# Kernel tuning notes

Measured on AMD Instinct MI355X. Metric: run time of the kernel, lower is better.

Reference implementation:

```python
import jax, jax.numpy as jnp
import numpy as np

B, S, H, L, NH, HD, V, FF, NC = 8, 512, 768, 12, 12, 64, 21128, 3072, 6
MAX_REL = 64
EPS = 1e-12


def rel_pos_table(seq_len, depth=HD, max_rel=MAX_REL):
    # NeZha functional (sinusoidal) relative-position embeddings, [S, S, depth]
    r = np.arange(seq_len)
    dist = np.clip(r[None, :] - r[:, None], -max_rel, max_rel) + max_rel
    vocab = 2 * max_rel + 1
    pos = np.arange(vocab)[:, None].astype(np.float32)
    i = np.arange(depth)[None, :]
    angle = pos / np.power(10000.0, (2 * (i // 2)) / float(depth))
    table = np.where(i % 2 == 0, np.sin(angle), np.cos(angle)).astype(np.float32)
    return jnp.asarray(table[dist])


def layer_norm(x, g, b):
    mu = jnp.mean(x, axis=-1, keepdims=True)
    var = jnp.mean(jnp.square(x - mu), axis=-1, keepdims=True)
    return (x - mu) * jax.lax.rsqrt(var + EPS) * g + b


def setup_inputs() -> dict:
    key = jax.random.key(0)
    ks = jax.random.split(key, 32)
    sd = 0.02
    d = {
        'input_ids': jax.random.randint(ks[0], (B, S), 0, V, dtype=jnp.int32),
        'attention_mask': jnp.ones((B, S), dtype=jnp.int32),
        'word_emb': sd * jax.random.normal(ks[1], (V, H), jnp.float32),
        'pos_emb': sd * jax.random.normal(ks[2], (S, H), jnp.float32),
        'type_emb': sd * jax.random.normal(ks[3], (2, H), jnp.float32),
        'ln_emb_g': jnp.ones((H,), jnp.float32),
        'ln_emb_b': jnp.zeros((H,), jnp.float32),
        'Wq': sd * jax.random.normal(ks[4], (L, H, H), jnp.float32),
        'bq': jnp.zeros((L, H), jnp.float32),
        'Wk': sd * jax.random.normal(ks[5], (L, H, H), jnp.float32),
        'bk': jnp.zeros((L, H), jnp.float32),
        'Wv': sd * jax.random.normal(ks[6], (L, H, H), jnp.float32),
        'bv': jnp.zeros((L, H), jnp.float32),
        'Wo': sd * jax.random.normal(ks[7], (L, H, H), jnp.float32),
        'bo': jnp.zeros((L, H), jnp.float32),
        'ln1_g': jnp.ones((L, H), jnp.float32),
        'ln1_b': jnp.zeros((L, H), jnp.float32),
        'W1': sd * jax.random.normal(ks[8], (L, H, FF), jnp.float32),
        'b1': jnp.zeros((L, FF), jnp.float32),
        'W2': sd * jax.random.normal(ks[9], (L, FF, H), jnp.float32),
        'b2': jnp.zeros((L, H), jnp.float32),
        'ln2_g': jnp.ones((L, H), jnp.float32),
        'ln2_b': jnp.zeros((L, H), jnp.float32),
        'pool_W': sd * jax.random.normal(ks[10], (H, H), jnp.float32),
        'pool_b': jnp.zeros((H,), jnp.float32),
        'cls_W': sd * jax.random.normal(ks[11], (2 * H, NC), jnp.float32),
        'cls_b': jnp.zeros((NC,), jnp.float32),
    }
    return d


def nezha_forward(input_ids, attention_mask, word_emb, pos_emb, type_emb,
                  ln_emb_g, ln_emb_b, Wq, bq, Wk, bk, Wv, bv, Wo, bo,
                  ln1_g, ln1_b, W1, b1, W2, b2, ln2_g, ln2_b,
                  pool_W, pool_b, cls_W, cls_b):
    seq = input_ids.shape[1]
    rel = rel_pos_table(seq)  # [S, S, HD], shared for keys and values
    mask_bias = (1.0 - attention_mask.astype(jnp.float32)) * -10000.0  # [B, S]

    x = word_emb[input_ids] + pos_emb[:seq][None, :, :] + type_emb[0][None, None, :]
    x = layer_norm(x, ln_emb_g, ln_emb_b)

    scale = 1.0 / jnp.sqrt(jnp.asarray(HD, jnp.float32))
    for l in range(L):
        q = (x @ Wq[l] + bq[l]).reshape(B, seq, NH, HD)
        k = (x @ Wk[l] + bk[l]).reshape(B, seq, NH, HD)
        v = (x @ Wv[l] + bv[l]).reshape(B, seq, NH, HD)
        # content scores + relative-position key scores
        scores = jnp.einsum('bihd,bjhd->bhij', q, k) + jnp.einsum('bihd,ijd->bhij', q, rel)
        scores = scores * scale + mask_bias[:, None, None, :]
        attn = jax.nn.softmax(scores, axis=-1)
        # content context + relative-position value context
        ctx = jnp.einsum('bhij,bjhd->bihd', attn, v) + jnp.einsum('bhij,ijd->bihd', attn, rel)
        ctx = ctx.reshape(B, seq, H)
        x = layer_norm(x + ctx @ Wo[l] + bo[l], ln1_g[l], ln1_b[l])
        h = jax.nn.gelu(x @ W1[l] + b1[l], approximate=False)
        x = layer_norm(x + h @ W2[l] + b2[l], ln2_g[l], ln2_b[l])

    pooled = jnp.tanh(x[:, 0] @ pool_W + pool_b)        # [B, H]
    seq_avg = jnp.mean(x, axis=1)                        # [B, H] (unmasked, as in torch.mean)
    concat = jnp.concatenate([seq_avg, pooled], axis=1)  # [B, 2H]
    return concat @ cls_W + cls_b                        # [B, 6]


def reference(input_ids, attention_mask, word_emb, pos_emb, type_emb,
              ln_emb_g, ln_emb_b, Wq, bq, Wk, bk, Wv, bv, Wo, bo,
              ln1_g, ln1_b, W1, b1, W2, b2, ln2_g, ln2_b,
              pool_W, pool_b, cls_W, cls_b):
    return nezha_forward(input_ids, attention_mask, word_emb, pos_emb, type_emb,
                         ln_emb_g, ln_emb_b, Wq, bq, Wk, bk, Wv, bv, Wo, bo,
                         ln1_g, ln1_b, W1, b1, W2, b2, ln2_g, ln2_b,
                         pool_W, pool_b, cls_W, cls_b)
```

## Files before the change

### kernel.cpp

```cpp
#include <hip/hip_runtime.h>
#include <hip/hip_bf16.h>
#include <math.h>

typedef __hip_bfloat16 bf;

#define B_ 8
#define S_ 512
#define H_ 768
#define L_ 12
#define NH_ 12
#define HD_ 64
#define FF_ 3072
#define NC_ 6
#define BS_ (B_ * S_)
#define BSH_ ((size_t)BS_ * H_)
#define KAUG_ 672
#define TAUG_ 160
#define TPAD_ 144
#define QSTR_ 2304

typedef __attribute__((ext_vector_type(8))) short s16x8;
typedef __attribute__((ext_vector_type(4))) float fx4;

__device__ __forceinline__ float LD(const void* p, size_t i, int isbf) {
    return isbf ? __bfloat162float(((const bf*)p)[i]) : ((const float*)p)[i];
}

__device__ __forceinline__ void gload16(const void* g, void* l) {
    __builtin_amdgcn_global_load_lds(
        (const __attribute__((address_space(1))) void*)g,
        (__attribute__((address_space(3))) void*)l, 16, 0, 0);
}

__device__ __forceinline__ s16x8 ldfrag64(const unsigned short* base, int row, int chunk) {
    return *(const s16x8*)((const char*)base + row * 128 + ((chunk ^ (row & 7)) << 4));
}
__device__ __forceinline__ s16x8 ldfrag32(const unsigned short* base, int row, int chunk) {
    return *(const s16x8*)((const char*)base + row * 64 + ((chunk ^ (row & 3)) << 4));
}

__device__ __forceinline__ float wred_sum(float v) {
#pragma unroll
    for (int o = 32; o; o >>= 1) v += __shfl_xor(v, o, 64);
    return v;
}
__device__ __forceinline__ float wred_max(float v) {
#pragma unroll
    for (int o = 32; o; o >>= 1) v = fmaxf(v, __shfl_xor(v, o, 64));
    return v;
}

__global__ void detect_kernel(const unsigned int* __restrict__ g, int* __restrict__ flag) {
    if (threadIdx.x == 0 && blockIdx.x == 0) {
        flag[0] = (g[0] == 0x3F800000u) ? 0 : 1;
        flag[1] = 0;
    }
}

__global__ void build_table_kernel(float* __restrict__ tab) {
    int idx = blockIdx.x * 256 + threadIdx.x;
    if (idx >= 129 * 64) return;
    int p = idx >> 6, d = idx & 63;
    double angle = (double)p / pow(10000.0, (double)(2 * (d / 2)) / 64.0);
    tab[idx] = (float)((d & 1) ? cos(angle) : sin(angle));
}

__global__ void build_tabT_kernel(const float* __restrict__ tab,
                                  bf* __restrict__ th, bf* __restrict__ tl) {
    int idx = blockIdx.x * 256 + threadIdx.x;
    if (idx >= 64 * TAUG_) return;
    int d = idx / TAUG_, t = idx % TAUG_;
    float v = (t < 129) ? tab[t * 64 + d] : 0.0f;
    bf h = __float2bfloat16(v);
    th[idx] = h;
    tl[idx] = __float2bfloat16(v - __bfloat162float(h));
}

__global__ void build_tabS_kernel(const float* __restrict__ tab,
                                  bf* __restrict__ th, bf* __restrict__ tl) {
    int idx = blockIdx.x * 256 + threadIdx.x;
    if (idx >= TPAD_ * 64) return;
    int t = idx >> 6;
    float v = (t < 129) ? tab[idx] : 0.0f;
    bf h = __float2bfloat16(v);
    th[idx] = h;
    tl[idx] = __float2bfloat16(v - __bfloat162float(h));
}

__global__ __launch_bounds__(256) void embed_kernel(
    const int* __restrict__ ids, const void* __restrict__ we,
    const void* __restrict__ pe, const void* __restrict__ te,
    float* __restrict__ y, const int* __restrict__ fl) {
    int isbf = *fl;
    int t = blockIdx.x;
    int s = t & (S_ - 1);
    int id = ids[t];
    size_t base = (size_t)t * H_;
    for (int c = threadIdx.x; c < H_; c += 256) {
        y[base + c] = LD(we, (size_t)id * H_ + c, isbf) +
                      LD(pe, (size_t)s * H_ + c, isbf) +
                      LD(te, c, isbf);
    }
}

__global__ void maskbias_kernel(const int* __restrict__ mask, float* __restrict__ mb) {
    int t = blockIdx.x * 256 + threadIdx.x;
    if (t < BS_) mb[t] = (1.0f - (float)mask[t]) * -10000.0f;
}

__global__ void biascat_kernel(const void* __restrict__ bq, const void* __restrict__ bk,
                               const void* __restrict__ bv, size_t off,
                               float* __restrict__ out, const int* __restrict__ fl) {
    int isbf = *fl;
    int t = blockIdx.x * 256 + threadIdx.x;
    if (t >= 3 * H_) return;
    const void* src = t < H_ ? bq : (t < 2 * H_ ? bk : bv);
    out[t] = LD(src, off + (t % H_), isbf);
}

__global__ __launch_bounds__(256) void ln_kernel(
    float* out, bf* ohi, bf* olo, const float* a, const float* resid,
    const void* __restrict__ g, const void* __restrict__ b, size_t goff,
    const int* __restrict__ fl) {
    const int isbf = *fl;
    const int lane = threadIdx.x & 63, wv = threadIdx.x >> 6;
    const int row = blockIdx.x * 4 + wv;
    const size_t base = (size_t)row * H_;
    float v[12];
#pragma unroll
    for (int e = 0; e < 12; ++e) {
        const int c = lane + e * 64;
        v[e] = a[base + c];
        if (resid) v[e] += resid[base + c];
    }
    float s = 0.0f;
#pragma unroll
    for (int e = 0; e < 12; ++e) s += v[e];
    const float mu = wred_sum(s) * (1.0f / (float)H_);
    float q = 0.0f;
#pragma unroll
    for (int e = 0; e < 12; ++e) { v[e] -= mu; q += v[e] * v[e]; }
    const float rs = 1.0f / sqrtf(wred_sum(q) * (1.0f / (float)H_) + 1e-12f);
#pragma unroll
    for (int e = 0; e < 12; ++e) {
        const int c = lane + e * 64;
        float o = v[e] * rs * LD(g, goff + c, isbf) + LD(b, goff + c, isbf);
        out[base + c] = o;
        if (ohi) {
            bf h = __float2bfloat16(o);
            ohi[base + c] = h;
            olo[base + c] = __float2bfloat16(o - __bfloat162float(h));
        }
    }
}

__global__ __launch_bounds__(256) void transpose_split_kernel(
    const void* __restrict__ W, size_t woff, bf* __restrict__ th, bf* __restrict__ tl,
    int K, int N, const int* __restrict__ fl) {
    __shared__ float s[32][33];
    const int isbf = *fl;
    const int tx = threadIdx.x & 31, ty = threadIdx.x >> 5;
    const int k0 = blockIdx.x * 32, n0 = blockIdx.y * 32;
#pragma unroll
    for (int i = 0; i < 4; ++i) {
        int k = k0 + ty + i * 8;
        s[ty + i * 8][tx] = LD(W, woff + (size_t)k * N + (n0 + tx), isbf);
    }
    __syncthreads();
#pragma unroll
    for (int i = 0; i < 4; ++i) {
        int n = n0 + ty + i * 8;
        float v = s[tx][ty + i * 8];
        bf h = __float2bfloat16(v);
        bf l = __float2bfloat16(v - __bfloat162float(h));
        th[(size_t)n * K + k0 + tx] = h;
        tl[(size_t)n * K + k0 + tx] = l;
    }
}

template<int MR>
__global__ __launch_bounds__(256, 2) void mgemm_kernel(
    const bf* __restrict__ Ah, const bf* __restrict__ Al,
    const bf* __restrict__ Bh, const bf* __restrict__ Bl,
    const void* __restrict__ bias, size_t boff,
    float* __restrict__ C, bf* __restrict__ Chi, bf* __restrict__ Clo,
    int N, int K, int act, int split_out, const int* __restrict__ fl) {
    __shared__ __align__(16) unsigned short Ahs[MR * 32][32];
    __shared__ __align__(16) unsigned short Als[MR * 32][32];
    __shared__ __align__(16) unsigned short Bhs[128][32];
    __shared__ __align__(16) unsigned short Bls[128][32];
    const int tid  = threadIdx.x;
    const int lane = tid & 63;
    const int wid  = tid >> 6;
    const int wr   = wid >> 1, wc = wid & 1;
    const int m0 = blockIdx.y * (MR * 32), n0 = blockIdx.x * 128;
    const int srow = lane >> 2;
    const int scol = (lane & 3) * 8;

    const fx4 fzero = {0.f, 0.f, 0.f, 0.f};
    fx4 acc[MR][4];
#pragma unroll
    for (int i = 0; i < MR; ++i)
#pragma unroll
        for (int j = 0; j < 4; ++j) acc[i][j] = fzero;

    for (int k0 = 0; k0 < K; k0 += 32) {
#pragma unroll
        for (int t = 0; t < MR / 2; ++t) {
            const int r = wid * (MR * 8) + t * 16;
            const size_t ga = (size_t)(m0 + r + srow) * K + (k0 + scol);
            gload16(Ah + ga, &Ahs[r][0]);
            gload16(Al + ga, &Als[r][0]);
        }
#pragma unroll
        for (int t = 0; t < 2; ++t) {
            const int r = wid * 32 + t * 16;
            const size_t gb = (size_t)(n0 + r + srow) * K + (k0 + scol);
            gload16(Bh + gb, &Bhs[r][0]);
            gload16(Bl + gb, &Bls[r][0]);
        }
        __syncthreads();

        const int fr = lane & 15;
        const int ko = (lane >> 4) * 8;
        s16x8 ah[MR], al[MR], bh[4], bl[4];
#pragma unroll
        for (int f = 0; f < MR; ++f) {
            ah[f] = *(const s16x8*)&Ahs[wr * (MR * 16) + f * 16 + fr][ko];
            al[f] = *(const s16x8*)&Als[wr * (MR * 16) + f * 16 + fr][ko];
        }
#pragma unroll
        for (int f = 0; f < 4; ++f) {
            bh[f] = *(const s16x8*)&Bhs[wc * 64 + f * 16 + fr][ko];
            bl[f] = *(const s16x8*)&Bls[wc * 64 + f * 16 + fr][ko];
        }
#pragma unroll
        for (int im = 0; im < MR; ++im)
#pragma unroll
            for (int in = 0; in < 4; ++in) {
                acc[im][in] = __builtin_amdgcn_mfma_f32_16x16x32_bf16(ah[im], bh[in], acc[im][in], 0, 0, 0);
                acc[im][in] = __builtin_amdgcn_mfma_f32_16x16x32_bf16(ah[im], bl[in], acc[im][in], 0, 0, 0);
                acc[im][in] = __builtin_amdgcn_mfma_f32_16x16x32_bf16(al[im], bh[in], acc[im][in], 0, 0, 0);
            }
        __syncthreads();
    }

    const int isbf = *fl;
    const int cr0 = m0 + wr * (MR * 16) + (lane >> 4) * 4;
    const int cc0 = n0 + wc * 64 + (lane & 15);
#pragma unroll
    for (int in = 0; in < 4; ++in) {
        const int col = cc0 + in * 16;
        const float bv = LD(bias, boff + col, isbf);
#pragma unroll
        for (int im = 0; im < MR; ++im) {
#pragma unroll
            for (int r = 0; r < 4; ++r) {
                const int row = cr0 + im * 16 + r;
                float v = acc[im][in][r] + bv;
                if (act) v = 0.5f * v * (1.0f + erff(v * 0.70710678118654752f));
                if (split_out) {
                    bf h = __float2bfloat16(v);
                    bf l = __float2bfloat16(v - __bfloat162float(h));
                    Chi[(size_t)row * N + col] = h;
                    Clo[(size_t)row * N + col] = l;
                } else {
                    C[(size_t)row * N + col] = v;
                }
            }
        }
    }
}

__global__ __launch_bounds__(256) void qrel_kernel(
    const bf* __restrict__ qh, const bf* __restrict__ ql,
    const bf* __restrict__ tabSh, const bf* __restrict__ tabSl,
    float* __restrict__ qrel, int astr, int b0) {
    const int tid = threadIdx.x, lane = tid & 63, wv = tid >> 6;
    const int rbase = blockIdx.x * 128;
    const int h = blockIdx.y;
    const int t0 = blockIdx.z * 48;
    const int fr = lane & 15, ko = (lane >> 4) * 8;
    const fx4 fz = {0.f, 0.f, 0.f, 0.f};
    fx4 acc[2][3];
#pragma unroll
    for (int m = 0; m < 2; ++m)
#pragma unroll
        for (int n = 0; n < 3; ++n) acc[m][n] = fz;
#pragma unroll
    for (int ks = 0; ks < 2; ++ks) {
        s16x8 a_h[2], a_l[2], b_h[3], b_l[3];
#pragma unroll
        for (int m = 0; m < 2; ++m) {
            const int row = rbase + wv * 32 + m * 16 + fr;
            const size_t ga = ((size_t)(b0 * S_) + row) * astr + h * 64 + ks * 32 + ko;
            a_h[m] = *(const s16x8*)(qh + ga);
            a_l[m] = *(const s16x8*)(ql + ga);
        }
#pragma unroll
        for (int n = 0; n < 3; ++n) {
            const int trow = t0 + n * 16 + fr;
            const size_t gb = (size_t)trow * 64 + ks * 32 + ko;
            b_h[n] = *(const s16x8*)(tabSh + gb);
            b_l[n] = *(const s16x8*)(tabSl + gb);
        }
#pragma unroll
        for (int m = 0; m < 2; ++m)
#pragma unroll
            for (int n = 0; n < 3; ++n) {
                acc[m][n] = __builtin_amdgcn_mfma_f32_16x16x32_bf16(a_h[m], b_h[n], acc[m][n], 0, 0, 0);
                acc[m][n] = __builtin_amdgcn_mfma_f32_16x16x32_bf16(a_h[m], b_l[n], acc[m][n], 0, 0, 0);
                acc[m][n] = __builtin_amdgcn_mfma_f32_16x16x32_bf16(a_l[m], b_h[n], acc[m][n], 0, 0, 0);
            }
    }
    const int rr = (lane >> 4) * 4, cc = lane & 15;
#pragma unroll
    for (int m = 0; m < 2; ++m)
#pragma unroll
        for (int n = 0; n < 3; ++n)
#pragma unroll
            for (int r = 0; r < 4; ++r) {
                const int row = rbase + wv * 32 + m * 16 + rr + r;
                const int t = t0 + n * 16 + cc;
                const int bb = row >> 9, ii = row & (S_ - 1);
                qrel[(((size_t)bb * NH_ + h) * S_ + ii) * TPAD_ + t] = acc[m][n][r];
            }
}

__global__ __launch_bounds__(256, 2) void qk_kernel(
    const bf* __restrict__ qh, const bf* __restrict__ ql,
    const bf* __restrict__ kh, const bf* __restrict__ kl,
    float* __restrict__ sc, int astr, int b0) {
    __shared__ __align__(16) unsigned short Qh[128][64];
    __shared__ __align__(16) unsigned short Ql_[128][64];
    __shared__ __align__(16) unsigned short Kh[128][64];
    __shared__ __align__(16) unsigned short Kl[128][64];
    const int tid = threadIdx.x, lane = tid & 63, wv = tid >> 6;
    const int j0 = blockIdx.x * 128, i0 = blockIdx.y * 128;
    const int h = blockIdx.z % NH_, bb = blockIdx.z / NH_;
    const int b = b0 + bb;
    const int srow = lane >> 3;
    const int schunk = (lane & 7) ^ (srow & 7);
#pragma unroll
    for (int t = 0; t < 4; ++t) {
        const int r = wv * 32 + t * 8;
        const size_t ga = (size_t)(b * S_ + i0 + r + srow) * astr + h * 64 + schunk * 8;
        const size_t gb = (size_t)(b * S_ + j0 + r + srow) * astr + h * 64 + schunk * 8;
        gload16(qh + ga, &Qh[r][0]);
        gload16(ql + ga, &Ql_[r][0]);
        gload16(kh + gb, &Kh[r][0]);
        gload16(kl + gb, &Kl[r][0]);
    }
    __syncthreads();
    const int fr = lane & 15, g = lane >> 4;
    const int wr = wv >> 1, wc = wv & 1;
    const fx4 fz = {0.f, 0.f, 0.f, 0.f};
    fx4 acc[4][4];
#pragma unroll
    for (int i = 0; i < 4; ++i)
#pragma unroll
        for (int j = 0; j < 4; ++j) acc[i][j] = fz;
#pragma unroll
    for (int ks = 0; ks < 2; ++ks) {
        s16x8 ah[4], al[4], bh[4], bl[4];
#pragma unroll
        for (int m = 0; m < 4; ++m) {
            const int row = wr * 64 + m * 16 + fr;
            ah[m] = ldfrag64(&Qh[0][0], row, ks * 4 + g);
            al[m] = ldfrag64(&Ql_[0][0], row, ks * 4 + g);
        }
#pragma unroll
        for (int n = 0; n < 4; ++n) {
            const int row = wc * 64 + n * 16 + fr;
            bh[n] = ldfrag64(&Kh[0][0], row, ks * 4 + g);
            bl[n] = ldfrag64(&Kl[0][0], row, ks * 4 + g);
        }
#pragma unroll
        for (int m = 0; m < 4; ++m)
#pragma unroll
            for (int n = 0; n < 4; ++n) {
                acc[m][n] = __builtin_amdgcn_mfma_f32_16x16x32_bf16(ah[m], bh[n], acc[m][n], 0, 0, 0);
                acc[m][n] = __builtin_amdgcn_mfma_f32_16x16x32_bf16(ah[m], bl[n], acc[m][n], 0, 0, 0);
                acc[m][n] = __builtin_amdgcn_mfma_f32_16x16x32_bf16(al[m], bh[n], acc[m][n], 0, 0, 0);
            }
    }
    const int rr = (lane >> 4) * 4, cc = lane & 15;
#pragma unroll
    for (int m = 0; m < 4; ++m)
#pragma unroll
        for (int n = 0; n < 4; ++n)
#pragma unroll
            for (int r = 0; r < 4; ++r) {
                const int ii = i0 + wr * 64 + m * 16 + rr + r;
                const int jj = j0 + wc * 64 + n * 16 + cc;
                sc[(((size_t)bb * NH_ + h) * S_ + ii) * S_ + jj] = acc[m][n][r];
            }
}

__global__ __launch_bounds__(256) void smrel_kernel(
    const float* __restrict__ scores, const float* __restrict__ qrel,
    const float* __restrict__ mb,
    bf* __restrict__ pah, bf* __restrict__ pal, int b0) {
    const int lane = threadIdx.x & 63;
    const int wv = threadIdx.x >> 6;
    const int i = blockIdx.x * 4 + wv;
    const int h = blockIdx.y, bb = blockIdx.z;
    const int b = b0 + bb;
    const size_t srow = ((size_t)bb * NH_ + h) * S_ + i;
    const size_t qbase = srow * TPAD_;

    float s[8];
    float lmax = -1e30f;
#pragma unroll
    for (int rep = 0; rep < 8; ++rep) {
        const int j = lane + rep * 64;
        int t = j - i; t = t < -64 ? -64 : (t > 64 ? 64 : t);
        float v = (scores[srow * S_ + j] + qrel[qbase + t + 64]) * 0.125f + mb[b * S_ + j];
        s[rep] = v;
        lmax = fmaxf(lmax, v);
    }
    const float mx = wred_max(lmax);
    float lsum = 0.0f;
#pragma unroll
    for (int rep = 0; rep < 8; ++rep) {
        s[rep] = expf(s[rep] - mx);
        lsum += s[rep];
    }
    const float inv = 1.0f / wred_sum(lsum);

    const size_t rowbase = srow * KAUG_;
#pragma unroll
    for (int e = 0; e < 3; ++e) {
        const int t = lane + e * 64;
        if (t < TAUG_) {
            pah[rowbase + 512 + t] = __float2bfloat16(0.0f);
            pal[rowbase + 512 + t] = __float2bfloat16(0.0f);
        }
    }
    float s_lo = 0.0f, s_hi = 0.0f;
#pragma unroll
    for (int rep = 0; rep < 8; ++rep) {
        const int j = lane + rep * 64;
        const float v = s[rep] * inv;
        bf hh = __float2bfloat16(v);
        pah[rowbase + j] = hh;
        pal[rowbase + j] = __float2bfloat16(v - __bfloat162float(hh));
        const int d = j - i;
        if (d <= -64) s_lo += s[rep];
        else if (d >= 64) s_hi += s[rep];
        else {
            pah[rowbase + 512 + d + 64] = hh;
            pal[rowbase + 512 + d + 64] = __float2bfloat16(v - __bfloat162float(hh));
        }
    }
    s_lo = wred_sum(s_lo);
    s_hi = wred_sum(s_hi);
    if (lane == 0) {
        float v0 = s_lo * inv;
        bf h0 = __float2bfloat16(v0);
        pah[rowbase + 512] = h0;
        pal[rowbase + 512] = __float2bfloat16(v0 - __bfloat162float(h0));
        float v1 = s_hi * inv;
        bf h1 = __float2bfloat16(v1);
        pah[rowbase + 512 + 128] = h1;
        pal[rowbase + 512 + 128] = __float2bfloat16(v1 - __bfloat162float(h1));
    }
}

__global__ __launch_bounds__(256) void vaug_kernel(
    const bf* __restrict__ vh, const bf* __restrict__ vl,
    const bf* __restrict__ tabTh, const bf* __restrict__ tabTl,
    bf* __restrict__ vah, bf* __restrict__ val_, int astr, int b0) {
    __shared__ unsigned short tile[64][71];
    const int h = blockIdx.x, pl = blockIdx.y, bb = blockIdx.z;
    const int b = b0 + bb;
    const bf* src  = pl ? vl : vh;
    bf*       dst  = pl ? val_ : vah;
    const bf* tsrc = pl ? tabTl : tabTh;
    const int tid = threadIdx.x;
    const size_t dbase = ((size_t)bb * NH_ + h) * 64;
    for (int j0 = 0; j0 < S_; j0 += 64) {
        for (int idx = tid; idx < 4096; idx += 256) {
            int jj = idx >> 6, d = idx & 63;
            tile[jj][d] = *(const unsigned short*)&src[(size_t)(b * S_ + j0 + jj) * astr + h * 64 + d];
        }
        __syncthreads();
        for (int idx = tid; idx < 4096; idx += 256) {
            int d = idx >> 6, jj = idx & 63;
            *(unsigned short*)&dst[(dbase + d) * KAUG_ + j0 + jj] = tile[jj][d];
        }
        __syncthreads();
    }
    for (int idx = tid; idx < 64 * TAUG_; idx += 256) {
        int d = idx / TAUG_, t = idx % TAUG_;
        *(unsigned short*)&dst[(dbase + d) * KAUG_ + 512 + t] =
            *(const unsigned short*)&tsrc[idx];
    }
}

__global__ __launch_bounds__(256, 2) void pv_kernel(
    const bf* __restrict__ pah, const bf* __restrict__ pal,
    const bf* __restrict__ vah, const bf* __restrict__ val_,
    bf* __restrict__ ch, bf* __restrict__ cl, int b0) {
    __shared__ __align__(16) unsigned short Ah[128][32];
    __shared__ __align__(16) unsigned short Al[128][32];
    __shared__ __align__(16) unsigned short Bh[64][32];
    __shared__ __align__(16) unsigned short Bl[64][32];
    const int tid = threadIdx.x, lane = tid & 63, wv = tid >> 6;
    const int h = blockIdx.x, i0 = blockIdx.y * 128, bb = blockIdx.z;
    const int b = b0 + bb;
    const int srow = lane >> 2;
    const int schunk = (lane & 3) ^ (srow & 3);
    const fx4 fz = {0.f, 0.f, 0.f, 0.f};
    fx4 acc[2][4];
#pragma unroll
    for (int m = 0; m < 2; ++m)
#pragma unroll
        for (int n = 0; n < 4; ++n) acc[m][n] = fz;

    for (int k0 = 0; k0 < KAUG_; k0 += 32) {
#pragma unroll
        for (int t = 0; t < 2; ++t) {
            const int r = wv * 32 + t * 16;
            const size_t ga = (((size_t)bb * NH_ + h) * S_ + i0 + r + srow) * KAUG_ + k0 + schunk * 8;
            gload16(pah + ga, &Ah[r][0]);
            gload16(pal + ga, &Al[r][0]);
        }
        {
            const int r = wv * 16;
            const size_t gb = (((size_t)bb * NH_ + h) * 64 + r + srow) * KAUG_ + k0 + schunk * 8;
            gload16(vah + gb, &Bh[r][0]);
            gload16(val_ + gb, &Bl[r][0]);
        }
        __syncthreads();
        const int fr = lane & 15, g = lane >> 4;
        s16x8 a_h[2], a_l[2], b_h[4], b_l[4];
#pragma unroll
        for (int m = 0; m < 2; ++m) {
            const int row = wv * 32 + m * 16 + fr;
            a_h[m] = ldfrag32(&Ah[0][0], row, g);
            a_l[m] = ldfrag32(&Al[0][0], row, g);
        }
#pragma unroll
        for (int n = 0; n < 4; ++n) {
            const int row = n * 16 + fr;
            b_h[n] = ldfrag32(&Bh[0][0], row, g);
            b_l[n] = ldfrag32(&Bl[0][0], row, g);
        }
// ... 29 lines not shown
    const void* __restrict__ pb, float* __restrict__ pooled,
    const int* __restrict__ fl) {
    int isbf = *fl;
    int b = blockIdx.x;
    const float* xr = x + (size_t)b * S_ * H_;
    for (int n = threadIdx.x; n < H_; n += 256) {
        float acc = LD(pb, n, isbf);
        for (int kx = 0; kx < H_; ++kx)
            acc += xr[kx] * LD(pW, (size_t)kx * H_ + n, isbf);
        pooled[b * H_ + n] = tanhf(acc);
    }
}

__global__ __launch_bounds__(256) void seqavg_kernel(
    const float* __restrict__ x, float* __restrict__ sa) {
    int b = blockIdx.x;
    for (int c = threadIdx.x; c < H_; c += 256) {
        float s = 0.0f;
        for (int j = 0; j < S_; ++j) s += x[((size_t)b * S_ + j) * H_ + c];
        sa[b * H_ + c] = s * (1.0f / (float)S_);
    }
}

__global__ void head_kernel(const float* __restrict__ sa, const float* __restrict__ pooled,
                            const void* __restrict__ cW, const void* __restrict__ cb,
                            void* __restrict__ out, const int* __restrict__ fl) {
    int isbf = *fl;
    int t = threadIdx.x;
    if (t >= B_ * NC_) return;
    int b = t / NC_, c = t % NC_;
    float acc = LD(cb, c, isbf);
    for (int kx = 0; kx < H_; ++kx)
        acc += sa[b * H_ + kx] * LD(cW, (size_t)kx * NC_ + c, isbf);
    for (int kx = 0; kx < H_; ++kx)
        acc += pooled[b * H_ + kx] * LD(cW, (size_t)(H_ + kx) * NC_ + c, isbf);
    if (isbf) ((bf*)out)[t] = __float2bfloat16(acc);
    else      ((float*)out)[t] = acc;
}

extern "C" void kernel_launch(void* const* d_in, const int* in_sizes, int n_in,
                              void* d_out, int out_size, void* d_ws, size_t ws_size,
                              hipStream_t stream) {
    (void)in_sizes; (void)n_in; (void)out_size;
    const int* ids   = (const int*)d_in[0];
    const int* amask = (const int*)d_in[1];
    const void* we  = d_in[2];
    const void* pe  = d_in[3];
    const void* te  = d_in[4];
    const void* lng = d_in[5];
    const void* lnb = d_in[6];
    const void* Wq  = d_in[7];
    const void* bq  = d_in[8];
    const void* Wk  = d_in[9];
    const void* bk  = d_in[10];
    const void* Wv  = d_in[11];
    const void* bv  = d_in[12];
    const void* Wo  = d_in[13];
    const void* bo  = d_in[14];
    const void* l1g = d_in[15];
    const void* l1b = d_in[16];
    const void* W1  = d_in[17];
    const void* b1  = d_in[18];
    const void* W2  = d_in[19];
    const void* b2  = d_in[20];
    const void* l2g = d_in[21];
    const void* l2b = d_in[22];
    const void* pW  = d_in[23];
    const void* pb  = d_in[24];
    const void* cW  = d_in[25];
    const void* cb  = d_in[26];

    char* cur = (char*)d_ws;
    auto alloc = [&](size_t bytes) -> char* {
        char* p = cur;
        cur += (bytes + 255) & ~(size_t)255;
        return p;
    };
    float* x    = (float*)alloc(BSH_ * 4);
    float* r0   = (float*)alloc(BSH_ * 4);
    float* r1f  = (float*)alloc(BSH_ * 4);
    float* r2f  = (float*)alloc(BSH_ * 4);
    float* r3f  = (float*)alloc(BSH_ * 4);
    float* z    = (float*)alloc(BSH_ * 4);
    float* tab  = (float*)alloc(129 * 64 * 4);
    float* mb   = (float*)alloc(BS_ * 4);
    float* pool = (float*)alloc(B_ * H_ * 4);
    float* sa   = (float*)alloc(B_ * H_ * 4);
    float* bqkv = (float*)alloc(3 * H_ * 4);
    bf* tabTh   = (bf*)alloc(64 * TAUG_ * 2);
    bf* tabTl   = (bf*)alloc(64 * TAUG_ * 2);
    bf* tabSh   = (bf*)alloc(TPAD_ * 64 * 2);
    bf* tabSl   = (bf*)alloc(TPAD_ * 64 * 2);
    int* flag   = (int*)alloc(256);
    int* zflag  = flag + 1;

    const size_t fixed = (size_t)(cur - (char*)d_ws);
    auto regA_sz = [&](int CB) {
        size_t wt = (size_t)2 * H_ * FF_ * 2;
        size_t qr = (size_t)CB * NH_ * S_ * TPAD_ * 4;
        return (wt > qr ? wt : qr);
    };
    auto regB_sz = [&](int CB) {
        size_t xs = (size_t)4 * BSH_;
        size_t sc = (size_t)CB * NH_ * S_ * S_ * 4;
        return (xs > sc ? xs : sc);
    };
    auto need = [&](int CB) {
        return fixed + regA_sz(CB) + regB_sz(CB)
             + (size_t)CB * NH_ * S_ * KAUG_ * 2 * 2
             + (size_t)CB * NH_ * 64 * KAUG_ * 2 * 2
             + 4096;
    };
    int CB = 8;
    while (CB > 1 && need(CB) > ws_size) CB >>= 1;

    char* regA = alloc(regA_sz(CB));
    char* regB = alloc(regB_sz(CB));
    bf* pah  = (bf*)alloc((size_t)CB * NH_ * S_ * KAUG_ * 2 * 2);
    bf* pal  = pah + (size_t)CB * NH_ * S_ * KAUG_;
    bf* vah  = (bf*)alloc((size_t)CB * NH_ * 64 * KAUG_ * 2 * 2);
    bf* val_ = vah + (size_t)CB * NH_ * 64 * KAUG_;

    bf*    wth   = (bf*)regA;
    bf*    wtl   = wth + (size_t)H_ * FF_;
    float* qrelb = (float*)regA;
    bf*    xh    = (bf*)regB;
    bf*    xl    = xh + BSH_;
    float* scb   = (float*)regB;

    bf* qkvh = (bf*)r1f;
    bf* qkvl = qkvh + (size_t)BS_ * QSTR_;
    bf* ch   = (bf*)r0;  bf* cl = ch + BSH_;
    bf* hbh  = (bf*)r0;
    bf* hbl  = (bf*)r2f;

    detect_kernel<<<1, 64, 0, stream>>>((const unsigned int*)lng, flag);
    build_table_kernel<<<(129 * 64 + 255) / 256, 256, 0, stream>>>(tab);
    build_tabT_kernel<<<(64 * TAUG_ + 255) / 256, 256, 0, stream>>>(tab, tabTh, tabTl);
    build_tabS_kernel<<<(TPAD_ * 64 + 255) / 256, 256, 0, stream>>>(tab, tabSh, tabSl);
    maskbias_kernel<<<(BS_ + 255) / 256, 256, 0, stream>>>(amask, mb);
    embed_kernel<<<BS_, 256, 0, stream>>>(ids, we, pe, te, r0, flag);
    ln_kernel<<<BS_ / 4, 256, 0, stream>>>(x, xh, xl, r0, nullptr, lng, lnb, 0, flag);

    dim3 tpHH(H_ / 32, H_ / 32);
    dim3 tpHF(H_ / 32, FF_ / 32);
    dim3 tpFH(FF_ / 32, H_ / 32);
    dim3 gQKV(3 * H_ / 128, BS_ / 128);
    dim3 gH64(H_ / 128, BS_ / 64);
    dim3 gF(FF_ / 128, BS_ / 128);
    dim3 gQR(CB * S_ / 128, NH_, 3);
    dim3 gVA(NH_, 2, CB);
    dim3 gQK(4, 4, NH_ * CB);
    dim3 gSM(S_ / 4, NH_, CB);
    dim3 gPV(NH_, 4, CB);

    for (int l = 0; l < L_; ++l) {
        const size_t oHH = (size_t)l * H_ * H_;
        const size_t oH  = (size_t)l * H_;
        const size_t oHF = (size_t)l * H_ * FF_;
        const size_t oF  = (size_t)l * FF_;

        transpose_split_kernel<<<tpHH, 256, 0, stream>>>(Wq, oHH, wth, wtl, H_, H_, flag);
        transpose_split_kernel<<<tpHH, 256, 0, stream>>>(Wk, oHH,
            wth + (size_t)H_ * H_, wtl + (size_t)H_ * H_, H_, H_, flag);
        transpose_split_kernel<<<tpHH, 256, 0, stream>>>(Wv, oHH,
            wth + (size_t)2 * H_ * H_, wtl + (size_t)2 * H_ * H_, H_, H_, flag);
        biascat_kernel<<<(3 * H_ + 255) / 256, 256, 0, stream>>>(bq, bk, bv, oH, bqkv, flag);
        mgemm_kernel<4><<<gQKV, 256, 0, stream>>>(xh, xl, wth, wtl, bqkv, 0,
            nullptr, qkvh, qkvl, QSTR_, H_, 0, 1, zflag);

        for (int b0 = 0; b0 < B_; b0 += CB) {
            qrel_kernel<<<gQR, 256, 0, stream>>>(qkvh, qkvl, tabSh, tabSl, qrelb, QSTR_, b0);
            vaug_kernel<<<gVA, 256, 0, stream>>>(qkvh + 2 * H_, qkvl + 2 * H_,
                tabTh, tabTl, vah, val_, QSTR_, b0);
            qk_kernel<<<gQK, 256, 0, stream>>>(qkvh, qkvl, qkvh + H_, qkvl + H_,
                scb, QSTR_, b0);
            smrel_kernel<<<gSM, 256, 0, stream>>>(scb, qrelb, mb, pah, pal, b0);
            pv_kernel<<<gPV, 256, 0, stream>>>(pah, pal, vah, val_, ch, cl, b0);
        }

        transpose_split_kernel<<<tpHH, 256, 0, stream>>>(Wo, oHH, wth, wtl, H_, H_, flag);
        mgemm_kernel<2><<<gH64, 256, 0, stream>>>(ch, cl, wth, wtl, bo, oH,
            z, nullptr, nullptr, H_, H_, 0, 0, flag);
        ln_kernel<<<BS_ / 4, 256, 0, stream>>>(x, xh, xl, z, x, l1g, l1b, oH, flag);

        transpose_split_kernel<<<tpHF, 256, 0, stream>>>(W1, oHF, wth, wtl, H_, FF_, flag);
        mgemm_kernel<4><<<gF, 256, 0, stream>>>(xh, xl, wth, wtl, b1, oF,
            nullptr, hbh, hbl, FF_, H_, 1, 1, flag);
        transpose_split_kernel<<<tpFH, 256, 0, stream>>>(W2, oHF, wth, wtl, FF_, H_, flag);
        mgemm_kernel<2><<<gH64, 256, 0, stream>>>(hbh, hbl, wth, wtl, b2, oH,
            z, nullptr, nullptr, H_, FF_, 0, 0, flag);
        ln_kernel<<<BS_ / 4, 256, 0, stream>>>(x, xh, xl, z, x, l2g, l2b, oH, flag);
    }

    pool_kernel<<<B_, 256, 0, stream>>>(x, pW, pb, pool, flag);
    seqavg_kernel<<<B_, 256, 0, stream>>>(x, sa);
    head_kernel<<<1, 64, 0, stream>>>(sa, pool, cW, cb, d_out, flag);
}
```

Baseline: 6.869 ms.

## Fuse QK scores with softmax, split-K output GEMMs, swizzle GEMM blocks

Merges the QK score kernel and the relative-position softmax kernel into one kernel that keeps a full 128x512 score tile in registers, so the fp32 score matrix is never written to and read back from global memory. Output-projection and FFN-down GEMMs switch to a two-way split-K with 128-row tiles, and the two partial sums are added inside the following layernorm. GEMM workgroups are swizzled. The Q/K/V transposes are batched into a single launch, and all layers' biases are concatenated once up front. The fused kernel needs 128KB of dynamic LDS and large register arrays at occupancy 1, and split-K adds an extra fp32 buffer read.

```diff
diff --git a/kernel.cpp b/kernel.cpp
--- a/kernel.cpp
+++ b/kernel.cpp
@@ -44,9 +44,15 @@
     for (int o = 32; o; o >>= 1) v += __shfl_xor(v, o, 64);
     return v;
 }
-__device__ __forceinline__ float wred_max(float v) {
-#pragma unroll
-    for (int o = 32; o; o >>= 1) v = fmaxf(v, __shfl_xor(v, o, 64));
+
+__device__ __forceinline__ float gred_max(float v) {
+#pragma unroll
+    for (int o = 1; o < 16; o <<= 1) v = fmaxf(v, __shfl_xor(v, o, 64));
+    return v;
+}
+__device__ __forceinline__ float gred_sum(float v) {
+#pragma unroll
+    for (int o = 1; o < 16; o <<= 1) v += __shfl_xor(v, o, 64);
     return v;
 }
 
@@ -109,17 +115,18 @@
 }
 
 __global__ void biascat_kernel(const void* __restrict__ bq, const void* __restrict__ bk,
-                               const void* __restrict__ bv, size_t off,
-                               float* __restrict__ out, const int* __restrict__ fl) {
+                               const void* __restrict__ bv, float* __restrict__ out,
+                               const int* __restrict__ fl) {
     int isbf = *fl;
     int t = blockIdx.x * 256 + threadIdx.x;
-    if (t >= 3 * H_) return;
-    const void* src = t < H_ ? bq : (t < 2 * H_ ? bk : bv);
-    out[t] = LD(src, off + (t % H_), isbf);
+    if (t >= L_ * 3 * H_) return;
+    int l = t / (3 * H_), p = t % (3 * H_);
+    const void* s = p < H_ ? bq : (p < 2 * H_ ? bk : bv);
+    out[t] = LD(s, (size_t)l * H_ + (p % H_), isbf);
 }
 
 __global__ __launch_bounds__(256) void ln_kernel(
-    float* out, bf* ohi, bf* olo, const float* a, const float* resid,
+    float* out, bf* ohi, bf* olo, const float* a, const float* a2, const float* resid,
     const void* __restrict__ g, const void* __restrict__ b, size_t goff,
     const int* __restrict__ fl) {
     const int isbf = *fl;
@@ -131,6 +138,7 @@
     for (int e = 0; e < 12; ++e) {
         const int c = lane + e * 64;
         v[e] = a[base + c];
+        if (a2) v[e] += a2[base + c];
         if (resid) v[e] += resid[base + c];
     }
     float s = 0.0f;
@@ -178,22 +186,59 @@
     }
 }
 
+__global__ __launch_bounds__(256) void transpose_split3_kernel(
+    const void* __restrict__ W0, const void* __restrict__ W1p, const void* __restrict__ W2p,
+    size_t woff, bf* __restrict__ th, bf* __restrict__ tl, const int* __restrict__ fl) {
+    __shared__ float s[32][33];
+    const int isbf = *fl;
+    const void* W = blockIdx.z == 0 ? W0 : (blockIdx.z == 1 ? W1p : W2p);
+    bf* tho = th + (size_t)blockIdx.z * H_ * H_;
+    bf* tlo = tl + (size_t)blockIdx.z * H_ * H_;
+    const int tx = threadIdx.x & 31, ty = threadIdx.x >> 5;
+    const int k0 = blockIdx.x * 32, n0 = blockIdx.y * 32;
+#pragma unroll
+    for (int i = 0; i < 4; ++i) {
+        int k = k0 + ty + i * 8;
+        s[ty + i * 8][tx] = LD(W, woff + (size_t)k * H_ + (n0 + tx), isbf);
+    }
+    __syncthreads();
+#pragma unroll
+    for (int i = 0; i < 4; ++i) {
+        int n = n0 + ty + i * 8;
+        float v = s[tx][ty + i * 8];
+        bf h = __float2bfloat16(v);
+        bf l = __float2bfloat16(v - __bfloat162float(h));
+        tho[(size_t)n * H_ + k0 + tx] = h;
+        tlo[(size_t)n * H_ + k0 + tx] = l;
+    }
+}
+
 template<int MR>
 __global__ __launch_bounds__(256, 2) void mgemm_kernel(
     const bf* __restrict__ Ah, const bf* __restrict__ Al,
     const bf* __restrict__ Bh, const bf* __restrict__ Bl,
     const void* __restrict__ bias, size_t boff,
-    float* __restrict__ C, bf* __restrict__ Chi, bf* __restrict__ Clo,
-    int N, int K, int act, int split_out, const int* __restrict__ fl) {
+    float* __restrict__ C, float* __restrict__ C2,
+    bf* __restrict__ Chi, bf* __restrict__ Clo,
+    int N, int K, int lda, int ldb, int act, int split_out, const int* __restrict__ fl) {
     __shared__ __align__(16) unsigned short Ahs[MR * 32][32];
     __shared__ __align__(16) unsigned short Als[MR * 32][32];
     __shared__ __align__(16) unsigned short Bhs[128][32];
     __shared__ __align__(16) unsigned short Bls[128][32];
+    const int gx = gridDim.x, gy = gridDim.y, gz = gridDim.z;
+    const int nwg = gx * gy * gz;
+    const int flat = (blockIdx.z * gy + blockIdx.y) * gx + blockIdx.x;
+    const int swz = (flat & 7) * (nwg >> 3) + (flat >> 3);
+    const int bx = swz % gx;
+    const int by = (swz / gx) % gy;
+    const int bz = swz / (gx * gy);
+
     const int tid  = threadIdx.x;
     const int lane = tid & 63;
     const int wid  = tid >> 6;
     const int wr   = wid >> 1, wc = wid & 1;
-    const int m0 = blockIdx.y * (MR * 32), n0 = blockIdx.x * 128;
+    const int m0 = by * (MR * 32), n0 = bx * 128;
+    const size_t koff = (size_t)bz * K;
     const int srow = lane >> 2;
     const int scol = (lane & 3) * 8;
 
@@ -208,14 +253,14 @@
 #pragma unroll
         for (int t = 0; t < MR / 2; ++t) {
             const int r = wid * (MR * 8) + t * 16;
-            const size_t ga = (size_t)(m0 + r + srow) * K + (k0 + scol);
+            const size_t ga = (size_t)(m0 + r + srow) * lda + koff + k0 + scol;
             gload16(Ah + ga, &Ahs[r][0]);
             gload16(Al + ga, &Als[r][0]);
         }
 #pragma unroll
         for (int t = 0; t < 2; ++t) {
             const int r = wid * 32 + t * 16;
-            const size_t gb = (size_t)(n0 + r + srow) * K + (k0 + scol);
+            const size_t gb = (size_t)(n0 + r + srow) * ldb + koff + k0 + scol;
             gload16(Bh + gb, &Bhs[r][0]);
             gload16(Bl + gb, &Bls[r][0]);
         }
@@ -246,12 +291,13 @@
     }
 
     const int isbf = *fl;
+    float* Co = (bz == 0) ? C : C2;
     const int cr0 = m0 + wr * (MR * 16) + (lane >> 4) * 4;
     const int cc0 = n0 + wc * 64 + (lane & 15);
 #pragma unroll
     for (int in = 0; in < 4; ++in) {
         const int col = cc0 + in * 16;
-        const float bv = LD(bias, boff + col, isbf);
+        const float bv = (bz == 0) ? LD(bias, boff + col, isbf) : 0.0f;
 #pragma unroll
         for (int im = 0; im < MR; ++im) {
 #pragma unroll
@@ -265,7 +311,7 @@
                     Chi[(size_t)row * N + col] = h;
                     Clo[(size_t)row * N + col] = l;
                 } else {
-                    C[(size_t)row * N + col] = v;
+                    Co[(size_t)row * N + col] = v;
                 }
             }
         }
@@ -327,143 +373,181 @@
             }
 }
 
-__global__ __launch_bounds__(256, 2) void qk_kernel(
+__global__ __launch_bounds__(512, 1) void qksm_kernel(
     const bf* __restrict__ qh, const bf* __restrict__ ql,
     const bf* __restrict__ kh, const bf* __restrict__ kl,
-    float* __restrict__ sc, int astr, int b0) {
-    __shared__ __align__(16) unsigned short Qh[128][64];
-    __shared__ __align__(16) unsigned short Ql_[128][64];
-    __shared__ __align__(16) unsigned short Kh[128][64];
-    __shared__ __align__(16) unsigned short Kl[128][64];
+    const float* __restrict__ qrel, const float* __restrict__ mb,
+    bf* __restrict__ pah, bf* __restrict__ pal, int astr, int b0) {
+    extern __shared__ __align__(16) char smem[];
+    unsigned short (*Kh_)[64] = (unsigned short(*)[64])smem;
+    unsigned short (*Kl_)[64] = (unsigned short(*)[64])(smem + 65536);
+    unsigned short (*P_)[512] = (unsigned short(*)[512])smem;
+    __shared__ float st_m[2][128], st_s[2][128], st_lo[2][128], st_hi[2][128];
+
     const int tid = threadIdx.x, lane = tid & 63, wv = tid >> 6;
-    const int j0 = blockIdx.x * 128, i0 = blockIdx.y * 128;
-    const int h = blockIdx.z % NH_, bb = blockIdx.z / NH_;
+    const int i0 = blockIdx.x * 128, h = blockIdx.y, bb = blockIdx.z;
     const int b = b0 + bb;
-    const int srow = lane >> 3;
-    const int schunk = (lane & 7) ^ (srow & 7);
-#pragma unroll
-    for (int t = 0; t < 4; ++t) {
-        const int r = wv * 32 + t * 8;
-        const size_t ga = (size_t)(b * S_ + i0 + r + srow) * astr + h * 64 + schunk * 8;
-        const size_t gb = (size_t)(b * S_ + j0 + r + srow) * astr + h * 64 + schunk * 8;
-        gload16(qh + ga, &Qh[r][0]);
-        gload16(ql + ga, &Ql_[r][0]);
-        gload16(kh + gb, &Kh[r][0]);
-        gload16(kl + gb, &Kl[r][0]);
-    }
+    const int rg = wv >> 1, hf = wv & 1;
+
+    const int srow = lane >> 3, schunk = (lane & 7) ^ (srow & 7);
+#pragma unroll
+    for (int t = 0; t < 8; ++t) {
+        const int r = wv * 64 + t * 8;
+        const size_t ga = (size_t)(b * S_ + r + srow) * astr + h * 64 + schunk * 8;
+        gload16(kh + ga, &Kh_[r][0]);
+        gload16(kl + ga, &Kl_[r][0]);
+    }
+    const int fr = lane & 15, gq = lane >> 4;
+    s16x8 a_h[2][2], a_l[2][2];
+#pragma unroll
+    for (int mm = 0; mm < 2; ++mm)
+#pragma unroll
+        for (int ks = 0; ks < 2; ++ks) {
+            const size_t ga = (size_t)(b * S_ + i0 + rg * 32 + mm * 16 + fr) * astr
+                            + h * 64 + ks * 32 + gq * 8;
+            a_h[mm][ks] = *(const s16x8*)(qh + ga);
+            a_l[mm][ks] = *(const s16x8*)(ql + ga);
+        }
     __syncthreads();
-    const int fr = lane & 15, g = lane >> 4;
-    const int wr = wv >> 1, wc = wv & 1;
+
     const fx4 fz = {0.f, 0.f, 0.f, 0.f};
-    fx4 acc[4][4];
-#pragma unroll
-    for (int i = 0; i < 4; ++i)
-#pragma unroll
-        for (int j = 0; j < 4; ++j) acc[i][j] = fz;
-#pragma unroll
-    for (int ks = 0; ks < 2; ++ks) {
-        s16x8 ah[4], al[4], bh[4], bl[4];
-#pragma unroll
-        for (int m = 0; m < 4; ++m) {
-            const int row = wr * 64 + m * 16 + fr;
-            ah[m] = ldfrag64(&Qh[0][0], row, ks * 4 + g);
-            al[m] = ldfrag64(&Ql_[0][0], row, ks * 4 + g);
-        }
-#pragma unroll
-        for (int n = 0; n < 4; ++n) {
-            const int row = wc * 64 + n * 16 + fr;
-            bh[n] = ldfrag64(&Kh[0][0], row, ks * 4 + g);
-            bl[n] = ldfrag64(&Kl[0][0], row, ks * 4 + g);
-        }
-#pragma unroll
-        for (int m = 0; m < 4; ++m)
-#pragma unroll
-            for (int n = 0; n < 4; ++n) {
-                acc[m][n] = __builtin_amdgcn_mfma_f32_16x16x32_bf16(ah[m], bh[n], acc[m][n], 0, 0, 0);
-                acc[m][n] = __builtin_amdgcn_mfma_f32_16x16x32_bf16(ah[m], bl[n], acc[m][n], 0, 0, 0);
-                acc[m][n] = __builtin_amdgcn_mfma_f32_16x16x32_bf16(al[m], bh[n], acc[m][n], 0, 0, 0);
-            }
-    }
-    const int rr = (lane >> 4) * 4, cc = lane & 15;
-#pragma unroll
-    for (int m = 0; m < 4; ++m)
-#pragma unroll
-        for (int n = 0; n < 4; ++n)
+    fx4 acc[2][16];
+#pragma unroll
+    for (int m = 0; m < 2; ++m)
+#pragma unroll
+        for (int n = 0; n < 16; ++n) acc[m][n] = fz;
+#pragma unroll
+    for (int nn = 0; nn < 16; ++nn) {
+        const int jrow = hf * 256 + nn * 16 + fr;
+#pragma unroll
+        for (int ks = 0; ks < 2; ++ks) {
+            const s16x8 b_h = ldfrag64(&Kh_[0][0], jrow, ks * 4 + gq);
+            const s16x8 b_l = ldfrag64(&Kl_[0][0], jrow, ks * 4 + gq);
+#pragma unroll
+            for (int mm = 0; mm < 2; ++mm) {
+                acc[mm][nn] = __builtin_amdgcn_mfma_f32_16x16x32_bf16(a_h[mm][ks], b_h, acc[mm][nn], 0, 0, 0);
+                acc[mm][nn] = __builtin_amdgcn_mfma_f32_16x16x32_bf16(a_h[mm][ks], b_l, acc[mm][nn], 0, 0, 0);
+                acc[mm][nn] = __builtin_amdgcn_mfma_f32_16x16x32_bf16(a_l[mm][ks], b_h, acc[mm][nn], 0, 0, 0);
+            }
+        }
+    }
+
+    const int c = lane & 15;
+    float m_w[2][4];
+#pragma unroll
+    for (int mm = 0; mm < 2; ++mm) {
+#pragma unroll
+        for (int r = 0; r < 4; ++r) {
+            const int row_l = rg * 32 + mm * 16 + gq * 4 + r;
+            const int ig = i0 + row_l;
+            const size_t qb = (((size_t)bb * NH_ + h) * S_ + ig) * TPAD_;
+            const float q0 = qrel[qb], q128 = qrel[qb + 128];
+            float mx = -1e30f;
+#pragma unroll
+            for (int nn = 0; nn < 16; ++nn) {
+                const int j = hf * 256 + nn * 16 + c;
+                const int d = j - ig;
+                const float qr = d <= -64 ? q0 : (d >= 64 ? q128 : qrel[qb + d + 64]);
+                const float v = (acc[mm][nn][r] + qr) * 0.125f + mb[b * S_ + j];
+                acc[mm][nn][r] = v;
+                mx = fmaxf(mx, v);
+            }
+            mx = gred_max(mx);
+            float sm = 0.0f, sl = 0.0f, sh = 0.0f;
+#pragma unroll
+            for (int nn = 0; nn < 16; ++nn) {
+                const int j = hf * 256 + nn * 16 + c;
+                const int d = j - ig;
+                const float e = expf(acc[mm][nn][r] - mx);
+                acc[mm][nn][r] = e;
+                sm += e;
+                if (d <= -64) sl += e;
+                else if (d >= 64) sh += e;
+            }
+            sm = gred_sum(sm); sl = gred_sum(sl); sh = gred_sum(sh);
+            m_w[mm][r] = mx;
+            if (c == 0) {
+                st_m[hf][row_l] = mx;
+                st_s[hf][row_l] = sm;
+                st_lo[hf][row_l] = sl;
+                st_hi[hf][row_l] = sh;
+            }
+        }
+    }
+    __syncthreads();
+
+    const size_t obase = ((size_t)bb * NH_ + h) * S_ + i0;
+#pragma unroll
+    for (int plane = 0; plane < 2; ++plane) {
+#pragma unroll
+        for (int mm = 0; mm < 2; ++mm)
 #pragma unroll
             for (int r = 0; r < 4; ++r) {
-                const int ii = i0 + wr * 64 + m * 16 + rr + r;
-                const int jj = j0 + wc * 64 + n * 16 + cc;
-                sc[(((size_t)bb * NH_ + h) * S_ + ii) * S_ + jj] = acc[m][n][r];
-            }
-}
-
-__global__ __launch_bounds__(256) void smrel_kernel(
-    const float* __restrict__ scores, const float* __restrict__ qrel,
-    const float* __restrict__ mb,
-    bf* __restrict__ pah, bf* __restrict__ pal, int b0) {
-    const int lane = threadIdx.x & 63;
-    const int wv = threadIdx.x >> 6;
-    const int i = blockIdx.x * 4 + wv;
-    const int h = blockIdx.y, bb = blockIdx.z;
-    const int b = b0 + bb;
-    const size_t srow = ((size_t)bb * NH_ + h) * S_ + i;
-    const size_t qbase = srow * TPAD_;
-
-    float s[8];
-    float lmax = -1e30f;
-#pragma unroll
-    for (int rep = 0; rep < 8; ++rep) {
-        const int j = lane + rep * 64;
-        int t = j - i; t = t < -64 ? -64 : (t > 64 ? 64 : t);
-        float v = (scores[srow * S_ + j] + qrel[qbase + t + 64]) * 0.125f + mb[b * S_ + j];
-        s[rep] = v;
-        lmax = fmaxf(lmax, v);
-    }
-    const float mx = wred_max(lmax);
-    float lsum = 0.0f;
-#pragma unroll
-    for (int rep = 0; rep < 8; ++rep) {
-        s[rep] = expf(s[rep] - mx);
-        lsum += s[rep];
-    }
-    const float inv = 1.0f / wred_sum(lsum);
-
-    const size_t rowbase = srow * KAUG_;
-#pragma unroll
-    for (int e = 0; e < 3; ++e) {
-        const int t = lane + e * 64;
-        if (t < TAUG_) {
-            pah[rowbase + 512 + t] = __float2bfloat16(0.0f);
-            pal[rowbase + 512 + t] = __float2bfloat16(0.0f);
-        }
-    }
-    float s_lo = 0.0f, s_hi = 0.0f;
-#pragma unroll
-    for (int rep = 0; rep < 8; ++rep) {
-        const int j = lane + rep * 64;
-        const float v = s[rep] * inv;
-        bf hh = __float2bfloat16(v);
-        pah[rowbase + j] = hh;
-        pal[rowbase + j] = __float2bfloat16(v - __bfloat162float(hh));
-        const int d = j - i;
-        if (d <= -64) s_lo += s[rep];
-        else if (d >= 64) s_hi += s[rep];
-        else {
-            pah[rowbase + 512 + d + 64] = hh;
-            pal[rowbase + 512 + d + 64] = __float2bfloat16(v - __bfloat162float(hh));
-        }
-    }
-    s_lo = wred_sum(s_lo);
-    s_hi = wred_sum(s_hi);
-    if (lane == 0) {
-        float v0 = s_lo * inv;
-        bf h0 = __float2bfloat16(v0);
-        pah[rowbase + 512] = h0;
-        pal[rowbase + 512] = __float2bfloat16(v0 - __bfloat162float(h0));
-        float v1 = s_hi * inv;
-        bf h1 = __float2bfloat16(v1);
-        pah[rowbase + 512 + 128] = h1;
-        pal[rowbase + 512 + 128] = __float2bfloat16(v1 - __bfloat162float(h1));
+                const int row_l = rg * 32 + mm * 16 + gq * 4 + r;
+                const float m0 = st_m[0][row_l], m1 = st_m[1][row_l];
+                const float M = fmaxf(m0, m1);
+                const float inv = 1.0f /
+                    (st_s[0][row_l] * expf(m0 - M) + st_s[1][row_l] * expf(m1 - M));
+                const float f = expf(m_w[mm][r] - M) * inv;
+#pragma unroll
+                for (int nn = 0; nn < 16; ++nn) {
+                    const int col = hf * 256 + nn * 16 + c;
+                    const float p = acc[mm][nn][r] * f;
+                    bf hb = __float2bfloat16(p);
+                    if (plane == 0) {
+                        P_[row_l][col] = *(unsigned short*)&hb;
+                    } else {
+                        const float lo = p - __bfloat162float(hb);
+                        bf lb = __float2bfloat16(lo);
+                        P_[row_l][col] = *(unsigned short*)&lb;
+                    }
+                }
+            }
+        __syncthreads();
+        bf* dst = plane == 0 ? pah : pal;
+#pragma unroll
+        for (int p = 0; p < 16; ++p) {
+            const int idx = tid + p * 512;
+            const int row = idx >> 6, ch = idx & 63;
+            const s16x8 v = *(const s16x8*)&P_[row][ch * 8];
+            *(s16x8*)((unsigned short*)dst + (obase + row) * KAUG_ + ch * 8) = v;
+        }
+#pragma unroll
+        for (int p = 0; p < 5; ++p) {
+            const int idx = tid + p * 512;
+            const int row = idx / 20, ach = idx % 20;
+            const float m0 = st_m[0][row], m1 = st_m[1][row];
+            const float M = fmaxf(m0, m1);
+            const float e0 = expf(m0 - M), e1 = expf(m1 - M);
+            const float inv = 1.0f / (st_s[0][row] * e0 + st_s[1][row] * e1);
+            unsigned short o[8] __attribute__((aligned(16)));
+#pragma unroll
+            for (int cc = 0; cc < 8; ++cc) {
+                const int t = ach * 8 + cc;
+                float v = 0.0f;
+                bool direct = false;
+                unsigned short dv = 0;
+                if (t == 0)        v = (st_lo[0][row] * e0 + st_lo[1][row] * e1) * inv;
+                else if (t == 128) v = (st_hi[0][row] * e0 + st_hi[1][row] * e1) * inv;
+                else if (t < 128) {
+                    const int c2 = i0 + row + t - 64;
+                    if (c2 >= 0 && c2 < 512) { dv = P_[row][c2]; direct = true; }
+                }
+                if (direct) o[cc] = dv;
+                else {
+                    bf hb = __float2bfloat16(v);
+                    if (plane == 0) o[cc] = *(unsigned short*)&hb;
+                    else {
+                        const float lo = v - __bfloat162float(hb);
+                        bf lb = __float2bfloat16(lo);
+                        o[cc] = *(unsigned short*)&lb;
+                    }
+                }
+            }
+            *(s16x8*)((unsigned short*)dst + (obase + row) * KAUG_ + 512 + ach * 8) =
+                *(const s16x8*)o;
+        }
+        __syncthreads();
     }
 }
 
@@ -659,11 +743,12 @@
     float* r2f  = (float*)alloc(BSH_ * 4);
     float* r3f  = (float*)alloc(BSH_ * 4);
     float* z    = (float*)alloc(BSH_ * 4);
+    float* z2   = (float*)alloc(BSH_ * 4);
     float* tab  = (float*)alloc(129 * 64 * 4);
     float* mb   = (float*)alloc(BS_ * 4);
     float* pool = (float*)alloc(B_ * H_ * 4);
     float* sa   = (float*)alloc(B_ * H_ * 4);
-    float* bqkv = (float*)alloc(3 * H_ * 4);
+    float* bqkv = (float*)alloc((size_t)L_ * 3 * H_ * 4);
     bf* tabTh   = (bf*)alloc(64 * TAUG_ * 2);
     bf* tabTl   = (bf*)alloc(64 * TAUG_ * 2);
     bf* tabSh   = (bf*)alloc(TPAD_ * 64 * 2);
@@ -677,13 +762,9 @@
         size_t qr = (size_t)CB * NH_ * S_ * TPAD_ * 4;
         return (wt > qr ? wt : qr);
     };
-    auto regB_sz = [&](int CB) {
-        size_t xs = (size_t)4 * BSH_;
-        size_t sc = (size_t)CB * NH_ * S_ * S_ * 4;
-        return (xs > sc ? xs : sc);
-    };
+    const size_t regB_bytes = (size_t)4 * BSH_;
     auto need = [&](int CB) {
-        return fixed + regA_sz(CB) + regB_sz(CB)
+        return fixed + regA_sz(CB) + regB_bytes
              + (size_t)CB * NH_ * S_ * KAUG_ * 2 * 2
              + (size_t)CB * NH_ * 64 * KAUG_ * 2 * 2
              + 4096;
@@ -692,7 +773,7 @@
     while (CB > 1 && need(CB) > ws_size) CB >>= 1;
 
     char* regA = alloc(regA_sz(CB));
-    char* regB = alloc(regB_sz(CB));
+    char* regB = alloc(regB_bytes);
     bf* pah  = (bf*)alloc((size_t)CB * NH_ * S_ * KAUG_ * 2 * 2);
     bf* pal  = pah + (size_t)CB * NH_ * S_ * KAUG_;
     bf* vah  = (bf*)alloc((size_t)CB * NH_ * 64 * KAUG_ * 2 * 2);
@@ -703,7 +784,6 @@
     float* qrelb = (float*)regA;
     bf*    xh    = (bf*)regB;
     bf*    xl    = xh + BSH_;
-    float* scb   = (float*)regB;
 
     bf* qkvh = (bf*)r1f;
     bf* qkvl = qkvh + (size_t)BS_ * QSTR_;
@@ -716,19 +796,20 @@
     build_tabT_kernel<<<(64 * TAUG_ + 255) / 256, 256, 0, stream>>>(tab, tabTh, tabTl);
     build_tabS_kernel<<<(TPAD_ * 64 + 255) / 256, 256, 0, stream>>>(tab, tabSh, tabSl);
     maskbias_kernel<<<(BS_ + 255) / 256, 256, 0, stream>>>(amask, mb);
+    biascat_kernel<<<(L_ * 3 * H_ + 255) / 256, 256, 0, stream>>>(bq, bk, bv, bqkv, flag);
     embed_kernel<<<BS_, 256, 0, stream>>>(ids, we, pe, te, r0, flag);
-    ln_kernel<<<BS_ / 4, 256, 0, stream>>>(x, xh, xl, r0, nullptr, lng, lnb, 0, flag);
-
+    ln_kernel<<<BS_ / 4, 256, 0, stream>>>(x, xh, xl, r0, nullptr, nullptr, lng, lnb, 0, flag);
+
+    dim3 tp3(H_ / 32, H_ / 32, 3);
     dim3 tpHH(H_ / 32, H_ / 32);
     dim3 tpHF(H_ / 32, FF_ / 32);
     dim3 tpFH(FF_ / 32, H_ / 32);
-    dim3 gQKV(3 * H_ / 128, BS_ / 128);
-    dim3 gH64(H_ / 128, BS_ / 64);
-    dim3 gF(FF_ / 128, BS_ / 128);
+    dim3 gQKV(3 * H_ / 128, BS_ / 128, 1);
+    dim3 gSK(H_ / 128, BS_ / 128, 2);
+    dim3 gF(FF_ / 128, BS_ / 128, 1);
     dim3 gQR(CB * S_ / 128, NH_, 3);
     dim3 gVA(NH_, 2, CB);
-    dim3 gQK(4, 4, NH_ * CB);
-    dim3 gSM(S_ / 4, NH_, CB);
+    dim3 gQS(S_ / 128, NH_, CB);
     dim3 gPV(NH_, 4, CB);
 
     for (int l = 0; l < L_; ++l) {
@@ -737,37 +818,32 @@
         const size_t oHF = (size_t)l * H_ * FF_;
         const size_t oF  = (size_t)l * FF_;
 
-        transpose_split_kernel<<<tpHH, 256, 0, stream>>>(Wq, oHH, wth, wtl, H_, H_, flag);
-        transpose_split_kernel<<<tpHH, 256, 0, stream>>>(Wk, oHH,
-            wth + (size_t)H_ * H_, wtl + (size_t)H_ * H_, H_, H_, flag);
-        transpose_split_kernel<<<tpHH, 256, 0, stream>>>(Wv, oHH,
-            wth + (size_t)2 * H_ * H_, wtl + (size_t)2 * H_ * H_, H_, H_, flag);
-        biascat_kernel<<<(3 * H_ + 255) / 256, 256, 0, stream>>>(bq, bk, bv, oH, bqkv, flag);
-        mgemm_kernel<4><<<gQKV, 256, 0, stream>>>(xh, xl, wth, wtl, bqkv, 0,
-            nullptr, qkvh, qkvl, QSTR_, H_, 0, 1, zflag);
+        transpose_split3_kernel<<<tp3, 256, 0, stream>>>(Wq, Wk, Wv, oHH, wth, wtl, flag);
+        mgemm_kernel<4><<<gQKV, 256, 0, stream>>>(xh, xl, wth, wtl,
+            bqkv, (size_t)l * 3 * H_, nullptr, nullptr, qkvh, qkvl,
+            QSTR_, H_, H_, H_, 0, 1, zflag);
 
         for (int b0 = 0; b0 < B_; b0 += CB) {
             qrel_kernel<<<gQR, 256, 0, stream>>>(qkvh, qkvl, tabSh, tabSl, qrelb, QSTR_, b0);
             vaug_kernel<<<gVA, 256, 0, stream>>>(qkvh + 2 * H_, qkvl + 2 * H_,
                 tabTh, tabTl, vah, val_, QSTR_, b0);
-            qk_kernel<<<gQK, 256, 0, stream>>>(qkvh, qkvl, qkvh + H_, qkvl + H_,
-                scb, QSTR_, b0);
-            smrel_kernel<<<gSM, 256, 0, stream>>>(scb, qrelb, mb, pah, pal, b0);
+            qksm_kernel<<<gQS, 512, 131072, stream>>>(qkvh, qkvl, qkvh + H_, qkvl + H_,
+                qrelb, mb, pah, pal, QSTR_, b0);
             pv_kernel<<<gPV, 256, 0, stream>>>(pah, pal, vah, val_, ch, cl, b0);
         }
 
         transpose_split_kernel<<<tpHH, 256, 0, stream>>>(Wo, oHH, wth, wtl, H_, H_, flag);
-        mgemm_kernel<2><<<gH64, 256, 0, stream>>>(ch, cl, wth, wtl, bo, oH,
-            z, nullptr, nullptr, H_, H_, 0, 0, flag);
-        ln_kernel<<<BS_ / 4, 256, 0, stream>>>(x, xh, xl, z, x, l1g, l1b, oH, flag);
+        mgemm_kernel<4><<<gSK, 256, 0, stream>>>(ch, cl, wth, wtl, bo, oH,
+            z, z2, nullptr, nullptr, H_, H_ / 2, H_, H_, 0, 0, flag);
+        ln_kernel<<<BS_ / 4, 256, 0, stream>>>(x, xh, xl, z, z2, x, l1g, l1b, oH, flag);
 
         transpose_split_kernel<<<tpHF, 256, 0, stream>>>(W1, oHF, wth, wtl, H_, FF_, flag);
         mgemm_kernel<4><<<gF, 256, 0, stream>>>(xh, xl, wth, wtl, b1, oF,
-            nullptr, hbh, hbl, FF_, H_, 1, 1, flag);
+            nullptr, nullptr, hbh, hbl, FF_, H_, H_, H_, 1, 1, flag);
         transpose_split_kernel<<<tpFH, 256, 0, stream>>>(W2, oHF, wth, wtl, FF_, H_, flag);
-        mgemm_kernel<2><<<gH64, 256, 0, stream>>>(hbh, hbl, wth, wtl, b2, oH,
-            z, nullptr, nullptr, H_, FF_, 0, 0, flag);
-        ln_kernel<<<BS_ / 4, 256, 0, stream>>>(x, xh, xl, z, x, l2g, l2b, oH, flag);
+        mgemm_kernel<4><<<gSK, 256, 0, stream>>>(hbh, hbl, wth, wtl, b2, oH,
+            z, z2, nullptr, nullptr, H_, FF_ / 2, FF_, FF_, 0, 0, flag);
+        ln_kernel<<<BS_ / 4, 256, 0, stream>>>(x, xh, xl, z, z2, x, l2g, l2b, oH, flag);
     }
 
     pool_kernel<<<B_, 256, 0, stream>>>(x, pW, pb, pool, flag);
```

Measured after the change: 6.690 ms. 1.03x faster.
